# Kernel optimization log

Hardware: AMD Instinct MI355X
Metric: run time of the kernel (lower is better)

The kernel has to match this reference:

```python
import jax, jax.numpy as jnp
import numpy as np


def _lstm_cell(x, h, c, W_ih, W_hh, b_ih, b_hh):
    # PyTorch LSTMCell: gates = x@W_ih^T + b_ih + h@W_hh^T + b_hh, order i,f,g,o
    gates = x @ W_ih.T + b_ih + h @ W_hh.T + b_hh
    i, f, g, o = jnp.split(gates, 4, axis=-1)
    c_new = jax.nn.sigmoid(f) * c + jax.nn.sigmoid(i) * jnp.tanh(g)
    h_new = jax.nn.sigmoid(o) * jnp.tanh(c_new)
    return h_new, c_new


def setup_inputs() -> dict:
    key = jax.random.key(0)
    ks = jax.random.split(key, 8)
    B, T, D, H = 64, 512, 256, 256  # input_size == rnn_hid_size (broadcast constraint)
    s = 1.0 / np.sqrt(H)
    return {
        "values": jax.random.normal(ks[0], (B, T, D), dtype=jnp.float32),
        "Deltas": jax.random.uniform(ks[1], (B, T, D), dtype=jnp.float32),
        "W_att": jax.random.uniform(ks[2], (D, D), minval=-s, maxval=s, dtype=jnp.float32),
        "b_att": jax.random.uniform(ks[3], (D,), minval=-s, maxval=s, dtype=jnp.float32),
        "W_ih": jax.random.uniform(ks[4], (4 * H, D), minval=-s, maxval=s, dtype=jnp.float32),
        "W_hh": jax.random.uniform(ks[5], (4 * H, H), minval=-s, maxval=s, dtype=jnp.float32),
        "b_ih": jax.random.uniform(ks[6], (4 * H,), minval=-s, maxval=s, dtype=jnp.float32),
        "b_hh": jax.random.uniform(ks[7], (4 * H,), minval=-s, maxval=s, dtype=jnp.float32),
    }


def reference(values, Deltas, W_att, b_att, W_ih, W_hh, b_ih, b_hh):
    B, T, D = values.shape
    H = W_hh.shape[1]
    # attention-transformed inputs (the LSTM consumes these, not raw values)
    vlin = values @ W_att.T + b_att                              # [B,T,D]
    # original computes bmm(vlin, values^T)[:, 0]; only row 0 is used
    a_tj = jax.nn.sigmoid(jnp.einsum('bd,btd->bt', vlin[:, 0], values))  # [B,T]
    Dc = jnp.cumsum(Deltas, axis=-2)                             # cumulative time gaps [B,T,D]

    h0 = jnp.zeros((B, H), dtype=values.dtype)
    c_zero = jnp.zeros((B, H), dtype=values.dtype)
    # t = 0: h updated, cell output stored in c_0, but carry c stays zeros (faithful quirk)
    h1, c_0 = _lstm_cell(vlin[:, 0], h0, c_zero, W_ih, W_hh, b_ih, b_hh)

    def step(carry, inp):
        h, c = carry
        x, a, d = inp                                            # [B,D], [B], [B,D]
        alpha = a[:, None] / jnp.log(jnp.e + d)                  # [B,H] since D == H
        c = alpha * c_0 + (1.0 - alpha) * c
        h, c = _lstm_cell(x, h, c, W_ih, W_hh, b_ih, b_hh)
        return (h, c), h

    xs = (jnp.swapaxes(vlin[:, 1:], 0, 1),   # [T-1,B,D]
          a_tj[:, 1:].T,                      # [T-1,B]
          jnp.swapaxes(Dc[:, 1:], 0, 1))     # [T-1,B,D]
    _, hs = jax.lax.scan(step, (h1, c_zero), xs)
    h_n = jnp.concatenate([h1[:, None], jnp.swapaxes(hs, 0, 1)], axis=1)  # [B,T,H]
    return h_n
```

## Files before the change

kernel.cpp:

```cpp
#include <hip/hip_runtime.h>
#include <math.h>

#define Bn 64
#define Tn 512
#define Dn 256
#define Hn 256
#define Gn 1024
#define KR 192
#define KL 64

typedef _Float16 f16x2 __attribute__((ext_vector_type(2)));
typedef short bf16x8 __attribute__((ext_vector_type(8)));
typedef float f32x4 __attribute__((ext_vector_type(4)));

union U32H2 { unsigned int u; f16x2 h; };

__device__ __forceinline__ f16x2 u2h(unsigned int u) { U32H2 v; v.u = u; return v.h; }
__device__ __forceinline__ unsigned int packh2(float x, float y) {
    U32H2 v; v.h = (f16x2){(_Float16)x, (_Float16)y}; return v.u;
}

__device__ __forceinline__ unsigned short f2bf(float x) {
    unsigned int u = __float_as_uint(x);
    u = u + 0x7FFFu + ((u >> 16) & 1u);
    return (unsigned short)(u >> 16);
}

#if __has_builtin(__builtin_amdgcn_fdot2)
__device__ __forceinline__ float fdot2f(f16x2 a, f16x2 b, float c) {
    return __builtin_amdgcn_fdot2(a, b, c, false);
}
#else
__device__ __forceinline__ float fdot2f(f16x2 a, f16x2 b, float c) {
    return fmaf((float)a[1], (float)b[1], fmaf((float)a[0], (float)b[0], c));
}
#endif

__device__ __forceinline__ float sigm(float x) {
    return __fdividef(1.0f, 1.0f + __expf(-x));
}
__device__ __forceinline__ float tanh_fast(float x) {
    float xc = fminf(fmaxf(x, -15.0f), 15.0f);
    float e = __expf(2.0f * xc);
    return 1.0f - __fdividef(2.0f, e + 1.0f);
}

__global__ void k_wc(const float* __restrict__ W_ih, const float* __restrict__ W_att,
                     const float* __restrict__ b_att, const float* __restrict__ b_ih,
                     const float* __restrict__ b_hh,
                     unsigned short* __restrict__ W_cb, float* __restrict__ bias_c) {
    int g = blockIdx.x;
    int k = threadIdx.x;
    __shared__ float wih_s[Dn];
    __shared__ float red[256];
    wih_s[k] = W_ih[g * Dn + k];
    __syncthreads();
    float acc = 0.0f;
    for (int d = 0; d < Dn; ++d)
        acc = fmaf(wih_s[d], W_att[d * Dn + k], acc);
    W_cb[g * Dn + k] = f2bf(acc);
    red[k] = wih_s[k] * b_att[k];
    __syncthreads();
    for (int s = 128; s > 0; s >>= 1) {
        if (k < s) red[k] += red[k + s];
        __syncthreads();
    }
    if (k == 0) bias_c[g] = red[0] + b_ih[g] + b_hh[g];
}

__global__ void k_vlin0(const float* __restrict__ values, const float* __restrict__ W_att,
                        const float* __restrict__ b_att, float* __restrict__ vlin0) {
    int b = blockIdx.x, d = threadIdx.x;
    __shared__ float v_s[Dn];
    v_s[d] = values[(size_t)b * Tn * Dn + d];
    __syncthreads();
    float acc = b_att[d];
    for (int k = 0; k < Dn; ++k)
        acc = fmaf(v_s[k], W_att[d * Dn + k], acc);
    vlin0[b * Dn + d] = acc;
}

__global__ void k_atj(const float* __restrict__ values, const float* __restrict__ vlin0,
                      float* __restrict__ a_tj) {
    int wid = threadIdx.x >> 6, lane = threadIdx.x & 63;
    int idx = blockIdx.x * 4 + wid;
    int b = idx >> 9;
    const float4* vp = (const float4*)(values + (size_t)idx * Dn);
    const float4* qp = (const float4*)(vlin0 + b * Dn);
    float4 v = vp[lane], q = qp[lane];
    float s = v.x * q.x + v.y * q.y + v.z * q.z + v.w * q.w;
    #pragma unroll
    for (int off = 32; off; off >>= 1) s += __shfl_xor(s, off);
    if (lane == 0) a_tj[idx] = 1.0f / (1.0f + expf(-s));
}

__global__ __launch_bounds__(256) void k_gemm(const float* __restrict__ A,
                                              const unsigned short* __restrict__ Bw,
                                              const float* __restrict__ bias,
                                              float* __restrict__ C) {
    __shared__ __align__(16) unsigned short As[128 * 32];
    __shared__ __align__(16) unsigned short Bs[128 * 32];
    const int tid = threadIdx.x;
    const int lane = tid & 63, wv = tid >> 6;
    const int wm = wv & 1, wn = wv >> 1;
    const int mBase = blockIdx.y * 128, nBase = blockIdx.x * 128;

    f32x4 acc[4][4];
    #pragma unroll
    for (int i = 0; i < 4; ++i)
        #pragma unroll
        for (int jj = 0; jj < 4; ++jj)
            acc[i][jj] = (f32x4){0.f, 0.f, 0.f, 0.f};

    for (int kb = 0; kb < 256; kb += 32) {
        #pragma unroll
        for (int p = 0; p < 2; ++p) {
            int idx = p * 256 + tid;
            int r = idx >> 2, c = idx & 3;
            const float* src = A + (size_t)(mBase + r) * 256 + kb + c * 8;
            float4 f0 = *(const float4*)src;
            float4 f1 = *(const float4*)(src + 4);
            bf16x8 v;
            v[0] = (short)f2bf(f0.x); v[1] = (short)f2bf(f0.y);
            v[2] = (short)f2bf(f0.z); v[3] = (short)f2bf(f0.w);
            v[4] = (short)f2bf(f1.x); v[5] = (short)f2bf(f1.y);
            v[6] = (short)f2bf(f1.z); v[7] = (short)f2bf(f1.w);
            int cs = c ^ ((r >> 1) & 3);
            *(bf16x8*)&As[r * 32 + cs * 8] = v;
        }
        #pragma unroll
        for (int p = 0; p < 2; ++p) {
            int idx = p * 256 + tid;
            int r = idx >> 2, c = idx & 3;
            bf16x8 v = *(const bf16x8*)(Bw + (size_t)(nBase + r) * 256 + kb + c * 8);
            int cs = c ^ ((r >> 1) & 3);
            *(bf16x8*)&Bs[r * 32 + cs * 8] = v;
        }
        __syncthreads();

        bf16x8 af[4], bfr[4];
        #pragma unroll
        for (int f = 0; f < 4; ++f) {
            int ra = wm * 64 + f * 16 + (lane & 15);
            int ca = (lane >> 4) ^ ((ra >> 1) & 3);
            af[f] = *(const bf16x8*)&As[ra * 32 + ca * 8];
            int rb = wn * 64 + f * 16 + (lane & 15);
            int cb = (lane >> 4) ^ ((rb >> 1) & 3);
            bfr[f] = *(const bf16x8*)&Bs[rb * 32 + cb * 8];
        }
        #pragma unroll
        for (int fm = 0; fm < 4; ++fm)
            #pragma unroll
            for (int fn = 0; fn < 4; ++fn)
                acc[fm][fn] = __builtin_amdgcn_mfma_f32_16x16x32_bf16(af[fm], bfr[fn], acc[fm][fn], 0, 0, 0);
        __syncthreads();
    }
    #pragma unroll
    for (int fm = 0; fm < 4; ++fm) {
        #pragma unroll
        for (int fn = 0; fn < 4; ++fn) {
            #pragma unroll
            for (int r = 0; r < 4; ++r) {
                int row = mBase + wm * 64 + fm * 16 + (lane >> 4) * 4 + r;
                int col = nBase + wn * 64 + fn * 16 + (lane & 15);
                C[(size_t)row * Gn + col] = acc[fm][fn][r] + bias[col];
            }
        }
    }
}

__global__ __attribute__((amdgpu_flat_work_group_size(512, 512), amdgpu_waves_per_eu(1, 1)))
void k_rec(const float* __restrict__ xW,
           const float* __restrict__ W_hh,
           const float* __restrict__ Deltas,
           const float* __restrict__ a_tj,
           float* __restrict__ out) {
    extern __shared__ __align__(16) char smem[];
    uint4*    Wl4  = (uint4*)smem;
    _Float16* hbuf = (_Float16*)(smem + 131072);

    const int tid = threadIdx.x;
    const int b = blockIdx.x;
    const int l = tid & 63;
    const int e = l >> 5;
    const int u = (tid >> 6) * 32 + (l & 31);
    const int rA = e * 512 + u;
    const int rB = rA + 256;

    f16x2 wa[96], wb[96];
    {
        const float4* pA = (const float4*)(W_hh + (size_t)rA * 256);
        const float4* pB = (const float4*)(W_hh + (size_t)rB * 256);
        #pragma unroll
        for (int q = 0; q < 48; ++q) {
            float4 v = pA[q];
            wa[2 * q + 0] = (f16x2){(_Float16)v.x, (_Float16)v.y};
            wa[2 * q + 1] = (f16x2){(_Float16)v.z, (_Float16)v.w};
            float4 w = pB[q];
            wb[2 * q + 0] = (f16x2){(_Float16)w.x, (_Float16)w.y};
            wb[2 * q + 1] = (f16x2){(_Float16)w.z, (_Float16)w.w};
        }
    }
    for (int idx = tid; idx < 8192; idx += 512) {
        int r = idx >> 3, c = idx & 7;
        const float* src = W_hh + (size_t)r * 256 + KR + c * 8;
        float4 f0 = *(const float4*)src;
        float4 f1 = *(const float4*)(src + 4);
        Wl4[c * 1024 + r] = (uint4){ packh2(f0.x, f0.y), packh2(f0.z, f0.w),
                                     packh2(f1.x, f1.y), packh2(f1.z, f1.w) };
    }

    float cst = 0.0f, c0, dcrun;

    {
        size_t xb = (size_t)b * Tn * Gn;
        float gA = xW[xb + rA];
        float gB = xW[xb + rB];
        float pA = __shfl_xor(gA, 32);
        float pB = __shfl_xor(gB, 32);
        float gi = e ? pA : gA;
        float gg = e ? gA : pA;
        float go = e ? gB : pB;
        dcrun = Deltas[(size_t)b * Tn * Dn + u];
        c0 = sigm(gi) * tanh_fast(gg);
        float h = sigm(go) * tanh_fast(c0);
        if (e == 0) {
            out[(size_t)b * Tn * Hn + u] = h;
            hbuf[u] = (_Float16)h;
        }
    }
    __syncthreads();

    #pragma unroll 1
    for (int t = 1; t < Tn; ++t) {
        size_t xb = ((size_t)b * Tn + t) * Gn;
        float xwA = xW[xb + rA];
        float xwB = xW[xb + rB];
        float del = Deltas[((size_t)b * Tn + t) * Dn + u];
        float at  = a_tj[b * Tn + t];

        const uint4* hp = (const uint4*)(hbuf + ((t + 1) & 1) * 256);
        float sA0 = 0.f, sA1 = 0.f, sB0 = 0.f, sB1 = 0.f;

        {
            const uint4* WlA = Wl4 + rA;
            const uint4* WlB = Wl4 + rB;
            #pragma unroll
            for (int c = 0; c < 8; ++c) {
                uint4 hv = hp[24 + c];
                uint4 wva = WlA[c * 1024];
                uint4 wvb = WlB[c * 1024];
                sA0 = fdot2f(u2h(wva.x), u2h(hv.x), sA0);
                sA1 = fdot2f(u2h(wva.y), u2h(hv.y), sA1);
                sA0 = fdot2f(u2h(wva.z), u2h(hv.z), sA0);
                sA1 = fdot2f(u2h(wva.w), u2h(hv.w), sA1);
                sB0 = fdot2f(u2h(wvb.x), u2h(hv.x), sB0);
                sB1 = fdot2f(u2h(wvb.y), u2h(hv.y), sB1);
                sB0 = fdot2f(u2h(wvb.z), u2h(hv.z), sB0);
                sB1 = fdot2f(u2h(wvb.w), u2h(hv.w), sB1);
            }
        }
        #pragma unroll
        for (int p = 0; p < 24; ++p) {
            uint4 hv = hp[p];
            f16x2 h0 = u2h(hv.x), h1 = u2h(hv.y), h2 = u2h(hv.z), h3 = u2h(hv.w);
            sA0 = fdot2f(wa[4 * p + 0], h0, sA0);
            sA1 = fdot2f(wa[4 * p + 1], h1, sA1);
            sA0 = fdot2f(wa[4 * p + 2], h2, sA0);
            sA1 = fdot2f(wa[4 * p + 3], h3, sA1);
            sB0 = fdot2f(wb[4 * p + 0], h0, sB0);
            sB1 = fdot2f(wb[4 * p + 1], h1, sB1);
            sB0 = fdot2f(wb[4 * p + 2], h2, sB0);
            sB1 = fdot2f(wb[4 * p + 3], h3, sB1);
        }

        float gA = xwA + sA0 + sA1;
        float gB = xwB + sB0 + sB1;
        float pA = __shfl_xor(gA, 32);
        float pB = __shfl_xor(gB, 32);
        float gi = e ? pA : gA;
        float gf = e ? pB : gB;
        float gg = e ? gA : pA;
        float go = e ? gB : pB;

        dcrun += del;
        float alpha = __fdividef(at, __logf(2.718281828459045f + dcrun));
        float cmix = alpha * c0 + (1.0f - alpha) * cst;
        cst = sigm(gf) * cmix + sigm(gi) * tanh_fast(gg);
        float h = sigm(go) * tanh_fast(cst);

        if (e == 0) {
            out[((size_t)b * Tn + t) * Hn + u] = h;
            hbuf[(t & 1) * 256 + u] = (_Float16)h;
        }
        asm volatile("s_waitcnt lgkmcnt(0)" ::: "memory");
        __builtin_amdgcn_s_barrier();
        __builtin_amdgcn_sched_barrier(0);
    }
}

extern "C" void kernel_launch(void* const* d_in, const int* in_sizes, int n_in,
                              void* d_out, int out_size, void* d_ws, size_t ws_size,
                              hipStream_t stream) {
    const float* values = (const float*)d_in[0];
    const float* Deltas = (const float*)d_in[1];
    const float* W_att  = (const float*)d_in[2];
    const float* b_att  = (const float*)d_in[3];
    const float* W_ih   = (const float*)d_in[4];
    const float* W_hh   = (const float*)d_in[5];
    const float* b_ih   = (const float*)d_in[6];
    const float* b_hh   = (const float*)d_in[7];
    float* out = (float*)d_out;

    float* xW = (float*)d_ws;
    unsigned short* W_cb = (unsigned short*)(xW + (size_t)32768 * 1024);
    float* bias_c = (float*)(W_cb + 1024 * 256);
    float* vlin0  = bias_c + 1024;
    float* atj    = vlin0 + 64 * 256;

    k_wc<<<1024, 256, 0, stream>>>(W_ih, W_att, b_att, b_ih, b_hh, W_cb, bias_c);
    k_vlin0<<<64, 256, 0, stream>>>(values, W_att, b_att, vlin0);
    k_atj<<<8192, 256, 0, stream>>>(values, vlin0, atj);
    k_gemm<<<dim3(8, 256), 256, 0, stream>>>(values, W_cb, bias_c, xW);
    k_rec<<<64, 512, 131072 + 1024, stream>>>(xW, W_hh, Deltas, atj, out);
}
```

Before: 1.150 ms.

## Use 256-thread recurrence with one hidden unit per thread and AGPR weight storage

The recurrent kernel now runs 256 threads per batch, each thread computing all four gates for one hidden unit. This removes the cross-lane shuffle exchange and the idle half of threads at output time. W_hh columns are split three ways: 80 in VGPRs, 128 held in AGPRs via inline asm constraints, and the remaining 48 in LDS, which shrinks shared memory use. The cost is 4x more dot-product work per thread and possible AGPR-to-VGPR copy overhead on the serial critical path.

```diff
diff --git a/kernel.cpp b/kernel.cpp
--- a/kernel.cpp
+++ b/kernel.cpp
@@ -6,8 +6,11 @@
 #define Dn 256
 #define Hn 256
 #define Gn 1024
-#define KR 192
-#define KL 64
+
+#define KA 80
+#define KG 128
+#define KLBASE (KA + KG)
+#define KLCH ((256 - KLBASE) / 8)
 
 typedef _Float16 f16x2 __attribute__((ext_vector_type(2)));
 typedef short bf16x8 __attribute__((ext_vector_type(8)));
@@ -169,7 +172,7 @@
     }
 }
 
-__global__ __attribute__((amdgpu_flat_work_group_size(512, 512), amdgpu_waves_per_eu(1, 1)))
+__global__ __attribute__((amdgpu_flat_work_group_size(256, 256), amdgpu_waves_per_eu(1, 1)))
 void k_rec(const float* __restrict__ xW,
            const float* __restrict__ W_hh,
            const float* __restrict__ Deltas,
@@ -177,33 +180,32 @@
            float* __restrict__ out) {
     extern __shared__ __align__(16) char smem[];
     uint4*    Wl4  = (uint4*)smem;
-    _Float16* hbuf = (_Float16*)(smem + 131072);
-
-    const int tid = threadIdx.x;
+    _Float16* hbuf = (_Float16*)(smem + KLCH * 1024 * 16);
+
+    const int j = threadIdx.x;
     const int b = blockIdx.x;
-    const int l = tid & 63;
-    const int e = l >> 5;
-    const int u = (tid >> 6) * 32 + (l & 31);
-    const int rA = e * 512 + u;
-    const int rB = rA + 256;
-
-    f16x2 wa[96], wb[96];
-    {
-        const float4* pA = (const float4*)(W_hh + (size_t)rA * 256);
-        const float4* pB = (const float4*)(W_hh + (size_t)rB * 256);
-        #pragma unroll
-        for (int q = 0; q < 48; ++q) {
-            float4 v = pA[q];
-            wa[2 * q + 0] = (f16x2){(_Float16)v.x, (_Float16)v.y};
-            wa[2 * q + 1] = (f16x2){(_Float16)v.z, (_Float16)v.w};
-            float4 w = pB[q];
-            wb[2 * q + 0] = (f16x2){(_Float16)w.x, (_Float16)w.y};
-            wb[2 * q + 1] = (f16x2){(_Float16)w.z, (_Float16)w.w};
-        }
-    }
-    for (int idx = tid; idx < 8192; idx += 512) {
-        int r = idx >> 3, c = idx & 7;
-        const float* src = W_hh + (size_t)r * 256 + KR + c * 8;
+
+    f16x2 wv[4][KA / 2];
+    unsigned wg[4][KG / 2];
+    #pragma unroll
+    for (int i = 0; i < 4; ++i) {
+        const float2* p2 = (const float2*)(W_hh + (size_t)(j + 256 * i) * 256);
+        #pragma unroll
+        for (int q = 0; q < KA / 2; ++q) {
+            float2 v = p2[q];
+            wv[i][q] = (f16x2){(_Float16)v.x, (_Float16)v.y};
+        }
+        #pragma unroll
+        for (int q = 0; q < KG / 2; ++q) {
+            float2 v = p2[KA / 2 + q];
+            unsigned pk = packh2(v.x, v.y);
+            asm volatile("" : "+a"(pk));
+            wg[i][q] = pk;
+        }
+    }
+    for (int idx = j; idx < KLCH * 1024; idx += 256) {
+        int c = idx >> 10, r = idx & 1023;
+        const float* src = W_hh + (size_t)r * 256 + KLBASE + c * 8;
         float4 f0 = *(const float4*)src;
         float4 f1 = *(const float4*)(src + 4);
         Wl4[c * 1024 + r] = (uint4){ packh2(f0.x, f0.y), packh2(f0.z, f0.w),
@@ -214,74 +216,72 @@
 
     {
         size_t xb = (size_t)b * Tn * Gn;
-        float gA = xW[xb + rA];
-        float gB = xW[xb + rB];
-        float pA = __shfl_xor(gA, 32);
-        float pB = __shfl_xor(gB, 32);
-        float gi = e ? pA : gA;
-        float gg = e ? gA : pA;
-        float go = e ? gB : pB;
-        dcrun = Deltas[(size_t)b * Tn * Dn + u];
+        float gi = xW[xb + j];
+        float gg = xW[xb + 512 + j];
+        float go = xW[xb + 768 + j];
+        dcrun = Deltas[(size_t)b * Tn * Dn + j];
         c0 = sigm(gi) * tanh_fast(gg);
         float h = sigm(go) * tanh_fast(c0);
-        if (e == 0) {
-            out[(size_t)b * Tn * Hn + u] = h;
-            hbuf[u] = (_Float16)h;
-        }
+        out[(size_t)b * Tn * Hn + j] = h;
+        hbuf[j] = (_Float16)h;
     }
     __syncthreads();
 
     #pragma unroll 1
     for (int t = 1; t < Tn; ++t) {
         size_t xb = ((size_t)b * Tn + t) * Gn;
-        float xwA = xW[xb + rA];
-        float xwB = xW[xb + rB];
-        float del = Deltas[((size_t)b * Tn + t) * Dn + u];
+        float xw0 = xW[xb + j];
+        float xw1 = xW[xb + 256 + j];
+        float xw2 = xW[xb + 512 + j];
+        float xw3 = xW[xb + 768 + j];
+        float del = Deltas[((size_t)b * Tn + t) * Dn + j];
         float at  = a_tj[b * Tn + t];
 
         const uint4* hp = (const uint4*)(hbuf + ((t + 1) & 1) * 256);
-        float sA0 = 0.f, sA1 = 0.f, sB0 = 0.f, sB1 = 0.f;
-
-        {
-            const uint4* WlA = Wl4 + rA;
-            const uint4* WlB = Wl4 + rB;
-            #pragma unroll
-            for (int c = 0; c < 8; ++c) {
-                uint4 hv = hp[24 + c];
-                uint4 wva = WlA[c * 1024];
-                uint4 wvb = WlB[c * 1024];
-                sA0 = fdot2f(u2h(wva.x), u2h(hv.x), sA0);
-                sA1 = fdot2f(u2h(wva.y), u2h(hv.y), sA1);
-                sA0 = fdot2f(u2h(wva.z), u2h(hv.z), sA0);
-                sA1 = fdot2f(u2h(wva.w), u2h(hv.w), sA1);
-                sB0 = fdot2f(u2h(wvb.x), u2h(hv.x), sB0);
-                sB1 = fdot2f(u2h(wvb.y), u2h(hv.y), sB1);
-                sB0 = fdot2f(u2h(wvb.z), u2h(hv.z), sB0);
-                sB1 = fdot2f(u2h(wvb.w), u2h(hv.w), sB1);
+        float s0[4] = {0.f, 0.f, 0.f, 0.f};
+        float s1[4] = {0.f, 0.f, 0.f, 0.f};
+
+        #pragma unroll
+        for (int c = 0; c < KLCH; ++c) {
+            uint4 hv = hp[KLBASE / 8 + c];
+            #pragma unroll
+            for (int i = 0; i < 4; ++i) {
+                uint4 w = Wl4[c * 1024 + j + 256 * i];
+                s0[i] = fdot2f(u2h(w.x), u2h(hv.x), s0[i]);
+                s1[i] = fdot2f(u2h(w.y), u2h(hv.y), s1[i]);
+                s0[i] = fdot2f(u2h(w.z), u2h(hv.z), s0[i]);
+                s1[i] = fdot2f(u2h(w.w), u2h(hv.w), s1[i]);
             }
         }
         #pragma unroll
-        for (int p = 0; p < 24; ++p) {
-            uint4 hv = hp[p];
+        for (int c = 0; c < KA / 8; ++c) {
+            uint4 hv = hp[c];
             f16x2 h0 = u2h(hv.x), h1 = u2h(hv.y), h2 = u2h(hv.z), h3 = u2h(hv.w);
-            sA0 = fdot2f(wa[4 * p + 0], h0, sA0);
-            sA1 = fdot2f(wa[4 * p + 1], h1, sA1);
-            sA0 = fdot2f(wa[4 * p + 2], h2, sA0);
-            sA1 = fdot2f(wa[4 * p + 3], h3, sA1);
-            sB0 = fdot2f(wb[4 * p + 0], h0, sB0);
-            sB1 = fdot2f(wb[4 * p + 1], h1, sB1);
-            sB0 = fdot2f(wb[4 * p + 2], h2, sB0);
-            sB1 = fdot2f(wb[4 * p + 3], h3, sB1);
-        }
-
-        float gA = xwA + sA0 + sA1;
-        float gB = xwB + sB0 + sB1;
-        float pA = __shfl_xor(gA, 32);
-        float pB = __shfl_xor(gB, 32);
-        float gi = e ? pA : gA;
-        float gf = e ? pB : gB;
-        float gg = e ? gA : pA;
-        float go = e ? gB : pB;
+            #pragma unroll
+            for (int i = 0; i < 4; ++i) {
+                s0[i] = fdot2f(wv[i][c * 4 + 0], h0, s0[i]);
+                s1[i] = fdot2f(wv[i][c * 4 + 1], h1, s1[i]);
+                s0[i] = fdot2f(wv[i][c * 4 + 2], h2, s0[i]);
+                s1[i] = fdot2f(wv[i][c * 4 + 3], h3, s1[i]);
+            }
+        }
+        #pragma unroll
+        for (int c = 0; c < KG / 8; ++c) {
+            uint4 hv = hp[KA / 8 + c];
+            f16x2 h0 = u2h(hv.x), h1 = u2h(hv.y), h2 = u2h(hv.z), h3 = u2h(hv.w);
+            #pragma unroll
+            for (int i = 0; i < 4; ++i) {
+                s0[i] = fdot2f(u2h(wg[i][c * 4 + 0]), h0, s0[i]);
+                s1[i] = fdot2f(u2h(wg[i][c * 4 + 1]), h1, s1[i]);
+                s0[i] = fdot2f(u2h(wg[i][c * 4 + 2]), h2, s0[i]);
+                s1[i] = fdot2f(u2h(wg[i][c * 4 + 3]), h3, s1[i]);
+            }
+        }
+
+        float gi = xw0 + s0[0] + s1[0];
+        float gf = xw1 + s0[1] + s1[1];
+        float gg = xw2 + s0[2] + s1[2];
+        float go = xw3 + s0[3] + s1[3];
 
         dcrun += del;
         float alpha = __fdividef(at, __logf(2.718281828459045f + dcrun));
@@ -289,14 +289,19 @@
         cst = sigm(gf) * cmix + sigm(gi) * tanh_fast(gg);
         float h = sigm(go) * tanh_fast(cst);
 
-        if (e == 0) {
-            out[((size_t)b * Tn + t) * Hn + u] = h;
-            hbuf[(t & 1) * 256 + u] = (_Float16)h;
-        }
+        out[((size_t)b * Tn + t) * Hn + j] = h;
+        hbuf[(t & 1) * 256 + j] = (_Float16)h;
+
         asm volatile("s_waitcnt lgkmcnt(0)" ::: "memory");
         __builtin_amdgcn_s_barrier();
         __builtin_amdgcn_sched_barrier(0);
     }
+
+    #pragma unroll
+    for (int i = 0; i < 4; ++i)
+        #pragma unroll
+        for (int q = 0; q < KG / 2; ++q)
+            asm volatile("" :: "a"(wg[i][q]));
 }
 
 extern "C" void kernel_launch(void* const* d_in, const int* in_sizes, int n_in,
@@ -322,5 +327,5 @@
     k_vlin0<<<64, 256, 0, stream>>>(values, W_att, b_att, vlin0);
     k_atj<<<8192, 256, 0, stream>>>(values, vlin0, atj);
     k_gemm<<<dim3(8, 256), 256, 0, stream>>>(values, W_cb, bias_c, xW);
-    k_rec<<<64, 512, 131072 + 1024, stream>>>(xW, W_hh, Deltas, atj, out);
-}
+    k_rec<<<64, 256, KLCH * 1024 * 16 + 1024, stream>>>(xW, W_hh, Deltas, atj, out);
+}
```

Result: slower. 2.504 ms (+117.7%).

## Split LSTM recurrence across four blocks per batch with global-memory h exchange

Applied to the files above, without the earlier changes.

Each batch element's recurrence is spread over 4 workgroups, each computing 64 hidden units with all W_hh weights held in registers instead of partly in LDS. Blocks exchange their packed f16 h slices every timestep through step-tagged 64-bit atomics in global memory, spin-waiting on the tag. Per-step inputs are prefetched one step ahead. This raises parallelism and shortens per-step dot products, at the cost of inter-block sync latency and reliance on all blocks being co-resident.

```diff
diff --git a/kernel.cpp b/kernel.cpp
--- a/kernel.cpp
+++ b/kernel.cpp
@@ -6,8 +6,6 @@
 #define Dn 256
 #define Hn 256
 #define Gn 1024
-#define KR 192
-#define KL 64
 
 typedef _Float16 f16x2 __attribute__((ext_vector_type(2)));
 typedef short bf16x8 __attribute__((ext_vector_type(8)));
@@ -169,119 +167,117 @@
     }
 }
 
-__global__ __attribute__((amdgpu_flat_work_group_size(512, 512), amdgpu_waves_per_eu(1, 1)))
+__global__ __launch_bounds__(512, 2)
 void k_rec(const float* __restrict__ xW,
            const float* __restrict__ W_hh,
            const float* __restrict__ Deltas,
            const float* __restrict__ a_tj,
+           unsigned long long* __restrict__ hglob,
            float* __restrict__ out) {
     extern __shared__ __align__(16) char smem[];
-    uint4*    Wl4  = (uint4*)smem;
-    _Float16* hbuf = (_Float16*)(smem + 131072);
+    unsigned* hbuf = (unsigned*)smem;
 
     const int tid = threadIdx.x;
-    const int b = blockIdx.x;
+    const int w = blockIdx.x;
+    const int q = (w >> 3) & 3;
+    const int b = (w & 7) * 8 + (w >> 5);
     const int l = tid & 63;
-    const int e = l >> 5;
-    const int u = (tid >> 6) * 32 + (l & 31);
-    const int rA = e * 512 + u;
-    const int rB = rA + 256;
-
-    f16x2 wa[96], wb[96];
+    const int Wv = tid >> 6;
+    const int vv = l >> 3;
+    const int gate = (l >> 1) & 3;
+    const int khalf = l & 1;
+    const int u = q * 64 + Wv * 8 + vv;
+    const int R = gate * 256 + u;
+
+    f16x2 wreg[64];
     {
-        const float4* pA = (const float4*)(W_hh + (size_t)rA * 256);
-        const float4* pB = (const float4*)(W_hh + (size_t)rB * 256);
-        #pragma unroll
-        for (int q = 0; q < 48; ++q) {
-            float4 v = pA[q];
-            wa[2 * q + 0] = (f16x2){(_Float16)v.x, (_Float16)v.y};
-            wa[2 * q + 1] = (f16x2){(_Float16)v.z, (_Float16)v.w};
-            float4 w = pB[q];
-            wb[2 * q + 0] = (f16x2){(_Float16)w.x, (_Float16)w.y};
-            wb[2 * q + 1] = (f16x2){(_Float16)w.z, (_Float16)w.w};
-        }
-    }
-    for (int idx = tid; idx < 8192; idx += 512) {
-        int r = idx >> 3, c = idx & 7;
-        const float* src = W_hh + (size_t)r * 256 + KR + c * 8;
-        float4 f0 = *(const float4*)src;
-        float4 f1 = *(const float4*)(src + 4);
-        Wl4[c * 1024 + r] = (uint4){ packh2(f0.x, f0.y), packh2(f0.z, f0.w),
-                                     packh2(f1.x, f1.y), packh2(f1.z, f1.w) };
-    }
-
+        const float4* wp = (const float4*)(W_hh + (size_t)R * 256 + khalf * 128);
+        #pragma unroll
+        for (int i = 0; i < 32; ++i) {
+            float4 v = wp[i];
+            wreg[2 * i]     = (f16x2){(_Float16)v.x, (_Float16)v.y};
+            wreg[2 * i + 1] = (f16x2){(_Float16)v.z, (_Float16)v.w};
+        }
+    }
+
+    const size_t xrow = (size_t)b * Tn;
     float cst = 0.0f, c0, dcrun;
+    float xw, del, at;
 
     {
-        size_t xb = (size_t)b * Tn * Gn;
-        float gA = xW[xb + rA];
-        float gB = xW[xb + rB];
-        float pA = __shfl_xor(gA, 32);
-        float pB = __shfl_xor(gB, 32);
-        float gi = e ? pA : gA;
-        float gg = e ? gA : pA;
-        float go = e ? gB : pB;
-        dcrun = Deltas[(size_t)b * Tn * Dn + u];
+        xw  = xW[xrow * Gn + R];
+        del = Deltas[xrow * Dn + u];
+        float Sr = xw;
+        float g2 = __shfl_xor(Sr, 2);
+        float p0 = (gate & 1) ? g2 : Sr;
+        float p1 = (gate & 1) ? Sr : g2;
+        float q0 = __shfl_xor(p0, 4);
+        float q1 = __shfl_xor(p1, 4);
+        float gi = (gate < 2) ? p0 : q0;
+        float gg = (gate < 2) ? q0 : p0;
+        float go = (gate < 2) ? q1 : p1;
+        dcrun = del;
         c0 = sigm(gi) * tanh_fast(gg);
         float h = sigm(go) * tanh_fast(c0);
-        if (e == 0) {
-            out[(size_t)b * Tn * Hn + u] = h;
-            hbuf[u] = (_Float16)h;
-        }
-    }
-    __syncthreads();
+        float hn = __shfl_xor(h, 8);
+        unsigned hpk = packh2(h, hn);
+        if ((l & 15) == 0) {
+            hbuf[u >> 1] = hpk;
+            unsigned long long pv = (1ull << 32) | (unsigned long long)hpk;
+            __hip_atomic_store(&hglob[((size_t)b * 2 + 0) * 128 + (u >> 1)], pv,
+                               __ATOMIC_RELAXED, __HIP_MEMORY_SCOPE_AGENT);
+        }
+        if ((l & 7) == 0) out[xrow * Hn + u] = h;
+        xw  = xW[(xrow + 1) * Gn + R];
+        del = Deltas[(xrow + 1) * Dn + u];
+        at  = a_tj[xrow + 1];
+    }
 
     #pragma unroll 1
     for (int t = 1; t < Tn; ++t) {
-        size_t xb = ((size_t)b * Tn + t) * Gn;
-        float xwA = xW[xb + rA];
-        float xwB = xW[xb + rB];
-        float del = Deltas[((size_t)b * Tn + t) * Dn + u];
-        float at  = a_tj[b * Tn + t];
-
-        const uint4* hp = (const uint4*)(hbuf + ((t + 1) & 1) * 256);
-        float sA0 = 0.f, sA1 = 0.f, sB0 = 0.f, sB1 = 0.f;
-
-        {
-            const uint4* WlA = Wl4 + rA;
-            const uint4* WlB = Wl4 + rB;
-            #pragma unroll
-            for (int c = 0; c < 8; ++c) {
-                uint4 hv = hp[24 + c];
-                uint4 wva = WlA[c * 1024];
-                uint4 wvb = WlB[c * 1024];
-                sA0 = fdot2f(u2h(wva.x), u2h(hv.x), sA0);
-                sA1 = fdot2f(u2h(wva.y), u2h(hv.y), sA1);
-                sA0 = fdot2f(u2h(wva.z), u2h(hv.z), sA0);
-                sA1 = fdot2f(u2h(wva.w), u2h(hv.w), sA1);
-                sB0 = fdot2f(u2h(wvb.x), u2h(hv.x), sB0);
-                sB1 = fdot2f(u2h(wvb.y), u2h(hv.y), sB1);
-                sB0 = fdot2f(u2h(wvb.z), u2h(hv.z), sB0);
-                sB1 = fdot2f(u2h(wvb.w), u2h(hv.w), sB1);
+        const int rb = (t - 1) & 1;
+        const int tn = (t + 1 < Tn) ? (t + 1) : t;
+        float xw_n  = xW[(xrow + tn) * Gn + R];
+        float del_n = Deltas[(xrow + tn) * Dn + u];
+        float at_n  = a_tj[xrow + tn];
+
+        if (tid < 96) {
+            const int pi = tid >> 5, off = tid & 31;
+            const int qp = pi + (pi >= q ? 1 : 0);
+            const unsigned long long* src =
+                &hglob[((size_t)b * 2 + rb) * 128 + qp * 32 + off];
+            unsigned long long v;
+            for (;;) {
+                v = __hip_atomic_load(src, __ATOMIC_RELAXED, __HIP_MEMORY_SCOPE_AGENT);
+                if ((unsigned)(v >> 32) == (unsigned)t) break;
+                __builtin_amdgcn_s_sleep(1);
             }
-        }
-        #pragma unroll
-        for (int p = 0; p < 24; ++p) {
-            uint4 hv = hp[p];
-            f16x2 h0 = u2h(hv.x), h1 = u2h(hv.y), h2 = u2h(hv.z), h3 = u2h(hv.w);
-            sA0 = fdot2f(wa[4 * p + 0], h0, sA0);
-            sA1 = fdot2f(wa[4 * p + 1], h1, sA1);
-            sA0 = fdot2f(wa[4 * p + 2], h2, sA0);
-            sA1 = fdot2f(wa[4 * p + 3], h3, sA1);
-            sB0 = fdot2f(wb[4 * p + 0], h0, sB0);
-            sB1 = fdot2f(wb[4 * p + 1], h1, sB1);
-            sB0 = fdot2f(wb[4 * p + 2], h2, sB0);
-            sB1 = fdot2f(wb[4 * p + 3], h3, sB1);
-        }
-
-        float gA = xwA + sA0 + sA1;
-        float gB = xwB + sB0 + sB1;
-        float pA = __shfl_xor(gA, 32);
-        float pB = __shfl_xor(gB, 32);
-        float gi = e ? pA : gA;
-        float gf = e ? pB : gB;
-        float gg = e ? gA : pA;
-        float go = e ? gB : pB;
+            hbuf[rb * 128 + qp * 32 + off] = (unsigned)v;
+        }
+        __syncthreads();
+
+        float s0 = 0.f, s1 = 0.f;
+        const uint4* hp = (const uint4*)(hbuf + rb * 128 + khalf * 64);
+        #pragma unroll
+        for (int cc = 0; cc < 16; ++cc) {
+            uint4 hv = hp[cc];
+            s0 = fdot2f(wreg[cc * 4 + 0], u2h(hv.x), s0);
+            s1 = fdot2f(wreg[cc * 4 + 1], u2h(hv.y), s1);
+            s0 = fdot2f(wreg[cc * 4 + 2], u2h(hv.z), s0);
+            s1 = fdot2f(wreg[cc * 4 + 3], u2h(hv.w), s1);
+        }
+        float Sr = s0 + s1;
+        Sr += __shfl_xor(Sr, 1);
+        Sr += xw;
+        float g2 = __shfl_xor(Sr, 2);
+        float p0 = (gate & 1) ? g2 : Sr;
+        float p1 = (gate & 1) ? Sr : g2;
+        float q0 = __shfl_xor(p0, 4);
+        float q1 = __shfl_xor(p1, 4);
+        float gi = (gate < 2) ? p0 : q0;
+        float gf = (gate < 2) ? p1 : q1;
+        float gg = (gate < 2) ? q0 : p0;
+        float go = (gate < 2) ? q1 : p1;
 
         dcrun += del;
         float alpha = __fdividef(at, __logf(2.718281828459045f + dcrun));
@@ -289,13 +285,18 @@
         cst = sigm(gf) * cmix + sigm(gi) * tanh_fast(gg);
         float h = sigm(go) * tanh_fast(cst);
 
-        if (e == 0) {
-            out[((size_t)b * Tn + t) * Hn + u] = h;
-            hbuf[(t & 1) * 256 + u] = (_Float16)h;
-        }
-        asm volatile("s_waitcnt lgkmcnt(0)" ::: "memory");
-        __builtin_amdgcn_s_barrier();
-        __builtin_amdgcn_sched_barrier(0);
+        float hn = __shfl_xor(h, 8);
+        unsigned hpk = packh2(h, hn);
+        if ((l & 15) == 0) {
+            hbuf[(t & 1) * 128 + (u >> 1)] = hpk;
+            unsigned long long pv =
+                ((unsigned long long)(unsigned)(t + 1) << 32) | (unsigned long long)hpk;
+            __hip_atomic_store(&hglob[((size_t)b * 2 + (t & 1)) * 128 + (u >> 1)], pv,
+                               __ATOMIC_RELAXED, __HIP_MEMORY_SCOPE_AGENT);
+        }
+        if ((l & 7) == 0) out[(xrow + t) * Hn + u] = h;
+
+        xw = xw_n; del = del_n; at = at_n;
     }
 }
 
@@ -312,15 +313,17 @@
     const float* b_hh   = (const float*)d_in[7];
     float* out = (float*)d_out;
 
-    float* xW = (float*)d_ws;
-    unsigned short* W_cb = (unsigned short*)(xW + (size_t)32768 * 1024);
-    float* bias_c = (float*)(W_cb + 1024 * 256);
-    float* vlin0  = bias_c + 1024;
-    float* atj    = vlin0 + 64 * 256;
+    char* wsb = (char*)d_ws;
+    float* xW            = (float*)(wsb);
+    unsigned short* W_cb = (unsigned short*)(wsb + 134217728);
+    float* bias_c        = (float*)(wsb + 134742016);
+    float* vlin0         = (float*)(wsb + 134746112);
+    float* atj           = (float*)(wsb + 134811648);
+    unsigned long long* hglob = (unsigned long long*)(wsb + 134942720);
 
     k_wc<<<1024, 256, 0, stream>>>(W_ih, W_att, b_att, b_ih, b_hh, W_cb, bias_c);
     k_vlin0<<<64, 256, 0, stream>>>(values, W_att, b_att, vlin0);
     k_atj<<<8192, 256, 0, stream>>>(values, vlin0, atj);
     k_gemm<<<dim3(8, 256), 256, 0, stream>>>(values, W_cb, bias_c, xW);
-    k_rec<<<64, 512, 131072 + 1024, stream>>>(xW, W_hh, Deltas, atj, out);
-}
+    k_rec<<<256, 512, 81920, stream>>>(xW, W_hh, Deltas, atj, hglob, out);
+}
```

Result: faster. 1.068 ms (-7.1%).

## Split recurrent matvec K across lane pairs with 1024 threads and LDS gate exchange

Applied to the files above, without the earlier changes.

The recurrent kernel moves from 512 to 1024 threads per block. Each lane pair now splits the K dimension of two W_hh rows, halving the per-thread register and LDS weight slice, and the partials are reduced with a lane shuffle. Gate pre-activations are written to an LDS buffer, and after an extra barrier 256 threads apply the cell update. This shortens the per-thread serial dot-product chain at the cost of a second block barrier per timestep and more LDS traffic.

```diff
diff --git a/kernel.cpp b/kernel.cpp
--- a/kernel.cpp
+++ b/kernel.cpp
@@ -6,8 +6,6 @@
 #define Dn 256
 #define Hn 256
 #define Gn 1024
-#define KR 192
-#define KL 64
 
 typedef _Float16 f16x2 __attribute__((ext_vector_type(2)));
 typedef short bf16x8 __attribute__((ext_vector_type(8)));
@@ -169,7 +167,7 @@
     }
 }
 
-__global__ __attribute__((amdgpu_flat_work_group_size(512, 512), amdgpu_waves_per_eu(1, 1)))
+__global__ __launch_bounds__(1024, 4)
 void k_rec(const float* __restrict__ xW,
            const float* __restrict__ W_hh,
            const float* __restrict__ Deltas,
@@ -177,22 +175,28 @@
            float* __restrict__ out) {
     extern __shared__ __align__(16) char smem[];
     uint4*    Wl4  = (uint4*)smem;
-    _Float16* hbuf = (_Float16*)(smem + 131072);
+    float*    gLDS = (float*)(smem + 131072);
+    unsigned* hbuf = (unsigned*)(smem + 131072 + 4160);
 
     const int tid = threadIdx.x;
     const int b = blockIdx.x;
     const int l = tid & 63;
-    const int e = l >> 5;
-    const int u = (tid >> 6) * 32 + (l & 31);
-    const int rA = e * 512 + u;
-    const int rB = rA + 256;
-
-    f16x2 wa[96], wb[96];
+    const int W = tid >> 6;
+    const int khalf = l & 1;
+    const int gate = (l >> 1) & 3;
+    const int grp = l >> 3;
+    const int u1 = W * 8 + grp;
+    const int u2 = u1 + 128;
+    const int Ra = gate * 256 + u1;
+    const int Rb = gate * 256 + u2;
+    const size_t xrow = (size_t)b * Tn;
+
+    f16x2 wa[48], wb[48];
     {
-        const float4* pA = (const float4*)(W_hh + (size_t)rA * 256);
-        const float4* pB = (const float4*)(W_hh + (size_t)rB * 256);
-        #pragma unroll
-        for (int q = 0; q < 48; ++q) {
+        const float4* pA = (const float4*)(W_hh + (size_t)Ra * 256) + khalf * 32;
+        const float4* pB = (const float4*)(W_hh + (size_t)Rb * 256) + khalf * 32;
+        #pragma unroll
+        for (int q = 0; q < 24; ++q) {
             float4 v = pA[q];
             wa[2 * q + 0] = (f16x2){(_Float16)v.x, (_Float16)v.y};
             wa[2 * q + 1] = (f16x2){(_Float16)v.z, (_Float16)v.w};
@@ -200,98 +204,99 @@
             wb[2 * q + 0] = (f16x2){(_Float16)w.x, (_Float16)w.y};
             wb[2 * q + 1] = (f16x2){(_Float16)w.z, (_Float16)w.w};
         }
-    }
-    for (int idx = tid; idx < 8192; idx += 512) {
-        int r = idx >> 3, c = idx & 7;
-        const float* src = W_hh + (size_t)r * 256 + KR + c * 8;
-        float4 f0 = *(const float4*)src;
-        float4 f1 = *(const float4*)(src + 4);
-        Wl4[c * 1024 + r] = (uint4){ packh2(f0.x, f0.y), packh2(f0.z, f0.w),
-                                     packh2(f1.x, f1.y), packh2(f1.z, f1.w) };
-    }
-
-    float cst = 0.0f, c0, dcrun;
-
-    {
-        size_t xb = (size_t)b * Tn * Gn;
-        float gA = xW[xb + rA];
-        float gB = xW[xb + rB];
-        float pA = __shfl_xor(gA, 32);
-        float pB = __shfl_xor(gB, 32);
-        float gi = e ? pA : gA;
-        float gg = e ? gA : pA;
-        float go = e ? gB : pB;
-        dcrun = Deltas[(size_t)b * Tn * Dn + u];
+        #pragma unroll
+        for (int c = 0; c < 4; ++c) {
+            float4 v0 = pA[24 + 2 * c], v1 = pA[24 + 2 * c + 1];
+            Wl4[c * 1024 + tid] = (uint4){ packh2(v0.x, v0.y), packh2(v0.z, v0.w),
+                                           packh2(v1.x, v1.y), packh2(v1.z, v1.w) };
+            float4 w0 = pB[24 + 2 * c], w1 = pB[24 + 2 * c + 1];
+            Wl4[(4 + c) * 1024 + tid] = (uint4){ packh2(w0.x, w0.y), packh2(w0.z, w0.w),
+                                                 packh2(w1.x, w1.y), packh2(w1.z, w1.w) };
+        }
+    }
+
+    float cst = 0.0f, c0 = 0.0f, dcrun = 0.0f;
+
+    if (tid < 256) {
+        float gi = xW[xrow * Gn + tid];
+        float gg = xW[xrow * Gn + 512 + tid];
+        float go = xW[xrow * Gn + 768 + tid];
+        dcrun = Deltas[xrow * Dn + tid];
         c0 = sigm(gi) * tanh_fast(gg);
         float h = sigm(go) * tanh_fast(c0);
-        if (e == 0) {
-            out[(size_t)b * Tn * Hn + u] = h;
-            hbuf[u] = (_Float16)h;
-        }
+        out[xrow * Hn + tid] = h;
+        float hn = __shfl_xor(h, 1);
+        if (!(tid & 1)) hbuf[tid >> 1] = packh2(h, hn);
     }
     __syncthreads();
 
     #pragma unroll 1
     for (int t = 1; t < Tn; ++t) {
-        size_t xb = ((size_t)b * Tn + t) * Gn;
-        float xwA = xW[xb + rA];
-        float xwB = xW[xb + rB];
-        float del = Deltas[((size_t)b * Tn + t) * Dn + u];
-        float at  = a_tj[b * Tn + t];
-
-        const uint4* hp = (const uint4*)(hbuf + ((t + 1) & 1) * 256);
-        float sA0 = 0.f, sA1 = 0.f, sB0 = 0.f, sB1 = 0.f;
-
-        {
-            const uint4* WlA = Wl4 + rA;
-            const uint4* WlB = Wl4 + rB;
-            #pragma unroll
-            for (int c = 0; c < 8; ++c) {
-                uint4 hv = hp[24 + c];
-                uint4 wva = WlA[c * 1024];
-                uint4 wvb = WlB[c * 1024];
-                sA0 = fdot2f(u2h(wva.x), u2h(hv.x), sA0);
-                sA1 = fdot2f(u2h(wva.y), u2h(hv.y), sA1);
-                sA0 = fdot2f(u2h(wva.z), u2h(hv.z), sA0);
-                sA1 = fdot2f(u2h(wva.w), u2h(hv.w), sA1);
-                sB0 = fdot2f(u2h(wvb.x), u2h(hv.x), sB0);
-                sB1 = fdot2f(u2h(wvb.y), u2h(hv.y), sB1);
-                sB0 = fdot2f(u2h(wvb.z), u2h(hv.z), sB0);
-                sB1 = fdot2f(u2h(wvb.w), u2h(hv.w), sB1);
-            }
-        }
-        #pragma unroll
-        for (int p = 0; p < 24; ++p) {
+        const size_t xb = (xrow + t) * Gn;
+        float xw_a = xW[xb + Ra];
+        float xw_b = xW[xb + Rb];
+        float del = 0.0f;
+        if (tid < 256) del = Deltas[(xrow + t) * Dn + tid];
+        float at = a_tj[xrow + t];
+
+        const uint4* hp = (const uint4*)(hbuf + ((t - 1) & 1) * 128 + khalf * 64);
+        float sa0 = 0.f, sa1 = 0.f, sb0 = 0.f, sb1 = 0.f;
+
+        #pragma unroll
+        for (int c = 0; c < 4; ++c) {
+            uint4 hv = hp[12 + c];
+            uint4 wA = Wl4[c * 1024 + tid];
+            uint4 wB = Wl4[(4 + c) * 1024 + tid];
+            sa0 = fdot2f(u2h(wA.x), u2h(hv.x), sa0);
+            sa1 = fdot2f(u2h(wA.y), u2h(hv.y), sa1);
+            sa0 = fdot2f(u2h(wA.z), u2h(hv.z), sa0);
+            sa1 = fdot2f(u2h(wA.w), u2h(hv.w), sa1);
+            sb0 = fdot2f(u2h(wB.x), u2h(hv.x), sb0);
+            sb1 = fdot2f(u2h(wB.y), u2h(hv.y), sb1);
+            sb0 = fdot2f(u2h(wB.z), u2h(hv.z), sb0);
+            sb1 = fdot2f(u2h(wB.w), u2h(hv.w), sb1);
+        }
+        #pragma unroll
+        for (int p = 0; p < 12; ++p) {
             uint4 hv = hp[p];
             f16x2 h0 = u2h(hv.x), h1 = u2h(hv.y), h2 = u2h(hv.z), h3 = u2h(hv.w);
-            sA0 = fdot2f(wa[4 * p + 0], h0, sA0);
-            sA1 = fdot2f(wa[4 * p + 1], h1, sA1);
-            sA0 = fdot2f(wa[4 * p + 2], h2, sA0);
-            sA1 = fdot2f(wa[4 * p + 3], h3, sA1);
-            sB0 = fdot2f(wb[4 * p + 0], h0, sB0);
-            sB1 = fdot2f(wb[4 * p + 1], h1, sB1);
-            sB0 = fdot2f(wb[4 * p + 2], h2, sB0);
-            sB1 = fdot2f(wb[4 * p + 3], h3, sB1);
-        }
-
-        float gA = xwA + sA0 + sA1;
-        float gB = xwB + sB0 + sB1;
-        float pA = __shfl_xor(gA, 32);
-        float pB = __shfl_xor(gB, 32);
-        float gi = e ? pA : gA;
-        float gf = e ? pB : gB;
-        float gg = e ? gA : pA;
-        float go = e ? gB : pB;
-
-        dcrun += del;
-        float alpha = __fdividef(at, __logf(2.718281828459045f + dcrun));
-        float cmix = alpha * c0 + (1.0f - alpha) * cst;
-        cst = sigm(gf) * cmix + sigm(gi) * tanh_fast(gg);
-        float h = sigm(go) * tanh_fast(cst);
-
-        if (e == 0) {
-            out[((size_t)b * Tn + t) * Hn + u] = h;
-            hbuf[(t & 1) * 256 + u] = (_Float16)h;
+            sa0 = fdot2f(wa[4 * p + 0], h0, sa0);
+            sa1 = fdot2f(wa[4 * p + 1], h1, sa1);
+            sa0 = fdot2f(wa[4 * p + 2], h2, sa0);
+            sa1 = fdot2f(wa[4 * p + 3], h3, sa1);
+            sb0 = fdot2f(wb[4 * p + 0], h0, sb0);
+            sb1 = fdot2f(wb[4 * p + 1], h1, sb1);
+            sb0 = fdot2f(wb[4 * p + 2], h2, sb0);
+            sb1 = fdot2f(wb[4 * p + 3], h3, sb1);
+        }
+
+        float Sa = sa0 + sa1;
+        float Sb = sb0 + sb1;
+        Sa += __shfl_xor(Sa, 1);
+        Sb += __shfl_xor(Sb, 1);
+        if (khalf == 0) {
+            gLDS[gate * 260 + u1] = Sa + xw_a;
+            gLDS[gate * 260 + u2] = Sb + xw_b;
+        }
+        asm volatile("s_waitcnt lgkmcnt(0)" ::: "memory");
+        __builtin_amdgcn_s_barrier();
+        __builtin_amdgcn_sched_barrier(0);
+
+        if (tid < 256) {
+            float gi = gLDS[tid];
+            float gf = gLDS[260 + tid];
+            float gg = gLDS[520 + tid];
+            float go = gLDS[780 + tid];
+
+            dcrun += del;
+            float alpha = __fdividef(at, __logf(2.718281828459045f + dcrun));
+            float cmix = alpha * c0 + (1.0f - alpha) * cst;
+            cst = sigm(gf) * cmix + sigm(gi) * tanh_fast(gg);
+            float h = sigm(go) * tanh_fast(cst);
+
+            out[(xrow + t) * Hn + tid] = h;
+            float hn = __shfl_xor(h, 1);
+            if (!(tid & 1)) hbuf[(t & 1) * 128 + (tid >> 1)] = packh2(h, hn);
         }
         asm volatile("s_waitcnt lgkmcnt(0)" ::: "memory");
         __builtin_amdgcn_s_barrier();
@@ -312,15 +317,16 @@
     const float* b_hh   = (const float*)d_in[7];
     float* out = (float*)d_out;
 
-    float* xW = (float*)d_ws;
-    unsigned short* W_cb = (unsigned short*)(xW + (size_t)32768 * 1024);
-    float* bias_c = (float*)(W_cb + 1024 * 256);
-    float* vlin0  = bias_c + 1024;
-    float* atj    = vlin0 + 64 * 256;
+    char* wsb = (char*)d_ws;
+    float* xW            = (float*)(wsb);
+    unsigned short* W_cb = (unsigned short*)(wsb + 134217728);
+    float* bias_c        = (float*)(wsb + 134742016);
+    float* vlin0         = (float*)(wsb + 134746112);
+    float* atj           = (float*)(wsb + 134811648);
 
     k_wc<<<1024, 256, 0, stream>>>(W_ih, W_att, b_att, b_ih, b_hh, W_cb, bias_c);
     k_vlin0<<<64, 256, 0, stream>>>(values, W_att, b_att, vlin0);
     k_atj<<<8192, 256, 0, stream>>>(values, vlin0, atj);
     k_gemm<<<dim3(8, 256), 256, 0, stream>>>(values, W_cb, bias_c, xW);
-    k_rec<<<64, 512, 131072 + 1024, stream>>>(xW, W_hh, Deltas, atj, out);
-}
+    k_rec<<<64, 1024, 131072 + 4160 + 1024, stream>>>(xW, W_hh, Deltas, atj, out);
+}
```

After: 1.252 ms. 8.8% more time.
